# Kernel optimization log

Hardware: AMD Instinct MI355X
Metric: run time of the kernel (lower is better)

## Reference

```python
import jax, jax.numpy as jnp
import numpy as np

B, N, DIM, NUM_NODE = 512, 64, 128, 43098
ALPHA = 0.2          # LeakyReLU negative slope (opt.alpha)
NEG_INF = -9e15      # mask value used by LocalAggregator


def setup_inputs() -> dict:
    key = jax.random.key(0)
    ks = jax.random.split(key, 6)
    stdv = 1.0 / np.sqrt(DIM)
    inputs = jax.random.randint(ks[0], (B, N), 0, NUM_NODE)
    adj = jax.random.randint(ks[1], (B, N, N), 0, 5)          # edge types 0..4
    mask_item = jax.random.randint(ks[2], (B, N), 0, 2)
    item = jax.random.randint(ks[3], (B, N), 0, NUM_NODE)
    embedding = jax.random.uniform(ks[4], (NUM_NODE, DIM), minval=-stdv, maxval=stdv, dtype=jnp.float32)
    attn_a = jax.random.uniform(ks[5], (4, DIM), minval=-stdv, maxval=stdv, dtype=jnp.float32)  # a_0..a_3
    return dict(inputs=inputs, adj=adj, mask_item=mask_item, item=item,
                embedding=embedding, attn_a=attn_a)


def _local_agg(h, adj, attn_a):
    # GCE-GNN LocalAggregator: a_input[b,i,j,:] = h[b,i,:]*h[b,j,:];
    # e_k[b,i,j] = leakyrelu(a_input @ a_k). Computed without materializing
    # the [B,N,N,D] tensor: e_k = leakyrelu(einsum over d of h_i*h_j*a_k).
    e = jax.nn.leaky_relu(jnp.einsum('kd,bid,bjd->kbij', attn_a, h, h), ALPHA)  # [4,B,N,N]
    alpha = jnp.full(e.shape[1:], NEG_INF, dtype=e.dtype)
    for k in range(4):  # edge-type masked selection: adj==k+1 -> e_k
        alpha = jnp.where(adj == k + 1, e[k], alpha)
    alpha = jax.nn.softmax(alpha, axis=-1)          # [B,N,N]
    return jnp.einsum('bij,bjd->bid', alpha, h)     # [B,N,D]


def reference(inputs, adj, mask_item, item, embedding, attn_a):
    h = embedding[inputs]                 # [B,N,D] embedding gather
    h_local = _local_agg(h, adj, attn_a)  # GAT-style local aggregation
    # F.dropout with training=False (eval/inference) is identity
    return h_local
```

## Files before the change

kernel.cpp:

```cpp
#include <hip/hip_runtime.h>
#include <hip/hip_bf16.h>


#define LRELU    0.2f

typedef __bf16 bf16x8 __attribute__((ext_vector_type(8)));
typedef float  f32x4  __attribute__((ext_vector_type(4)));

union FragU { bf16x8 v; unsigned u[4]; uint4 q; };

__device__ __forceinline__ unsigned pk2(float lo, float hi) {
  __hip_bfloat162 t = __float22bfloat162_rn(float2{lo, hi});
  unsigned u;
  __builtin_memcpy(&u, &t, 4);
  return u;
}
__device__ __forceinline__ float bflo(unsigned u) { return __builtin_bit_cast(float, u << 16); }
__device__ __forceinline__ float bfhi(unsigned u) { return __builtin_bit_cast(float, u & 0xffff0000u); }

__global__ __launch_bounds__(512, 4)
void cg_kernel(const int* __restrict__ inputs, const int* __restrict__ adj,
               const float* __restrict__ embedding, const float* __restrict__ attn_a,
               float* __restrict__ out) {
  __shared__ unsigned short Hb[64 * 128];
  __shared__ unsigned short HbT[128 * 64];
  __shared__ unsigned short HA[2][64 * 128];
  __shared__ unsigned short Pl[64 * 64];
  __shared__ float aaL[512];
  __shared__ float redS[64 * 2];

  const int b   = blockIdx.x;
  const int tid = threadIdx.x;
  const int w   = tid >> 6;
  const int l   = tid & 63;
  const int lr  = l & 15;
  const int lg  = l >> 4;
  const int it  = w >> 1;
  const int jh  = w & 1;

  char* HbB  = (char*)Hb;
  char* HbTB = (char*)HbT;
  char* PlB  = (char*)Pl;

  const int row = tid >> 3;
  const int c   = tid & 7;
  const int idx = inputs[b * 64 + row];

  int adjv[2][4];
#pragma unroll
  for (int jt2 = 0; jt2 < 2; ++jt2)
#pragma unroll
    for (int r = 0; r < 4; ++r)
      adjv[jt2][r] = adj[b * 4096 + (16 * it + 4 * lg + r) * 64 + 32 * jh + 16 * jt2 + lr];

  const float4* src = (const float4*)(embedding + (long)idx * 128 + c * 16);
  float4 v0 = src[0], v1 = src[1], v2 = src[2], v3 = src[3];
  aaL[tid] = attn_a[tid];

  unsigned pk[8];
  pk[0] = pk2(v0.x, v0.y); pk[1] = pk2(v0.z, v0.w);
  pk[2] = pk2(v1.x, v1.y); pk[3] = pk2(v1.z, v1.w);
  pk[4] = pk2(v2.x, v2.y); pk[5] = pk2(v2.z, v2.w);
  pk[6] = pk2(v3.x, v3.y); pk[7] = pk2(v3.z, v3.w);
  const int rswz = (row & 7) << 4;
  *(uint4*)(HbB + ((row * 256 + c * 32)      ^ rswz)) = uint4{pk[0], pk[1], pk[2], pk[3]};
  *(uint4*)(HbB + ((row * 256 + c * 32 + 16) ^ rswz)) = uint4{pk[4], pk[5], pk[6], pk[7]};
#pragma unroll
  for (int s = 0; s < 16; ++s) {
    int e = (s + 3 * c) & 15;
    int d = c * 16 + e;
    unsigned short hv = (unsigned short)((e & 1) ? (pk[e >> 1] >> 16) : (pk[e >> 1] & 0xffffu));
    *(unsigned short*)(HbTB + ((d * 128 + row * 2) ^ ((d & 7) << 4))) = hv;
  }
  float hf[16];
#pragma unroll
  for (int e = 0; e < 8; ++e) { hf[2 * e] = bflo(pk[e]); hf[2 * e + 1] = bfhi(pk[e]); }
  __syncthreads();

  uint4 bfrE[2][4];
#pragma unroll
  for (int jt2 = 0; jt2 < 2; ++jt2) {
    int jrow = 16 * (2 * jh + jt2) + lr;
#pragma unroll
    for (int kc = 0; kc < 4; ++kc)
      bfrE[jt2][kc] = *(const uint4*)(HbB + ((jrow * 256 + (kc * 32 + lg * 8) * 2) ^ ((jrow & 7) << 4)));
  }

  {
    float4 a0 = *(const float4*)&aaL[c * 16];
    float4 a1 = *(const float4*)&aaL[c * 16 + 4];
    float4 a2 = *(const float4*)&aaL[c * 16 + 8];
    float4 a3 = *(const float4*)&aaL[c * 16 + 12];
    char* HAB = (char*)HA[0];
    *(uint4*)(HAB + ((row * 256 + c * 32) ^ rswz)) =
        uint4{pk2(hf[0] * a0.x, hf[1] * a0.y),  pk2(hf[2] * a0.z, hf[3] * a0.w),
              pk2(hf[4] * a1.x, hf[5] * a1.y),  pk2(hf[6] * a1.z, hf[7] * a1.w)};
    *(uint4*)(HAB + ((row * 256 + c * 32 + 16) ^ rswz)) =
        uint4{pk2(hf[8] * a2.x,  hf[9] * a2.y),  pk2(hf[10] * a2.z, hf[11] * a2.w),
              pk2(hf[12] * a3.x, hf[13] * a3.y), pk2(hf[14] * a3.z, hf[15] * a3.w)};
  }
  __syncthreads();

  f32x4 acc[4][2];
#pragma unroll
  for (int k = 0; k < 4; ++k)
#pragma unroll
    for (int jt2 = 0; jt2 < 2; ++jt2) acc[k][jt2] = f32x4{0.f, 0.f, 0.f, 0.f};

#pragma unroll
  for (int k = 0; k < 4; ++k) {
    char* HAcur = (char*)HA[k & 1];
    if (k < 3) {
      float4 a0 = *(const float4*)&aaL[(k + 1) * 128 + c * 16];
      float4 a1 = *(const float4*)&aaL[(k + 1) * 128 + c * 16 + 4];
      float4 a2 = *(const float4*)&aaL[(k + 1) * 128 + c * 16 + 8];
      float4 a3 = *(const float4*)&aaL[(k + 1) * 128 + c * 16 + 12];
      char* HAnxt = (char*)HA[(k + 1) & 1];
      *(uint4*)(HAnxt + ((row * 256 + c * 32) ^ rswz)) =
          uint4{pk2(hf[0] * a0.x, hf[1] * a0.y),  pk2(hf[2] * a0.z, hf[3] * a0.w),
                pk2(hf[4] * a1.x, hf[5] * a1.y),  pk2(hf[6] * a1.z, hf[7] * a1.w)};
      *(uint4*)(HAnxt + ((row * 256 + c * 32 + 16) ^ rswz)) =
          uint4{pk2(hf[8] * a2.x,  hf[9] * a2.y),  pk2(hf[10] * a2.z, hf[11] * a2.w),
                pk2(hf[12] * a3.x, hf[13] * a3.y), pk2(hf[14] * a3.z, hf[15] * a3.w)};
    }
#pragma unroll
    for (int kc = 0; kc < 4; ++kc) {
      int arow = 16 * it + lr;
      FragU afr;
      afr.q = *(const uint4*)(HAcur + ((arow * 256 + (kc * 32 + lg * 8) * 2) ^ ((lr & 7) << 4)));
#pragma unroll
      for (int jt2 = 0; jt2 < 2; ++jt2) {
        FragU bfr; bfr.q = bfrE[jt2][kc];
        acc[k][jt2] = __builtin_amdgcn_mfma_f32_16x16x32_bf16(afr.v, bfr.v, acc[k][jt2], 0, 0, 0);
      }
    }
    if (k < 3) __syncthreads();
  }

  float p[2][4];
#pragma unroll
  for (int jt2 = 0; jt2 < 2; ++jt2)
#pragma unroll
    for (int r = 0; r < 4; ++r) {
      int av = adjv[jt2][r];
      float s = acc[0][jt2][r];
      s = (av == 2) ? acc[1][jt2][r] : s;
      s = (av == 3) ? acc[2][jt2][r] : s;
      s = (av == 4) ? acc[3][jt2][r] : s;
      float sl = s > 0.f ? s : LRELU * s;
      p[jt2][r] = (av != 0) ? __expf(sl) : 0.f;
    }
#pragma unroll
  for (int r = 0; r < 4; ++r) {
    int i = 16 * it + 4 * lg + r;
    int iswz = (i & 7) << 4;
    *(unsigned short*)(PlB + ((i * 128 + (32 * jh + lr) * 2)      ^ iswz)) = (unsigned short)(pk2(p[0][r], p[0][r]) & 0xffffu);
    *(unsigned short*)(PlB + ((i * 128 + (32 * jh + 16 + lr) * 2) ^ iswz)) = (unsigned short)(pk2(p[1][r], p[1][r]) & 0xffffu);
    float ss = p[0][r] + p[1][r];
    ss += __shfl_xor(ss, 1);
    ss += __shfl_xor(ss, 2);
    ss += __shfl_xor(ss, 4);
    ss += __shfl_xor(ss, 8);
    if (lr == 0) redS[i * 2 + jh] = ss;
  }
  __syncthreads();
  float z4[4];
#pragma unroll
  for (int r = 0; r < 4; ++r) {
    int i = 16 * it + 4 * lg + r;
    z4[r] = redS[i * 2] + redS[i * 2 + 1];
  }

  FragU afrP[2];
#pragma unroll
  for (int kc2 = 0; kc2 < 2; ++kc2) {
    int prow = 16 * it + lr;
    afrP[kc2].q = *(const uint4*)(PlB + ((prow * 128 + (kc2 * 32 + lg * 8) * 2) ^ ((lr & 7) << 4)));
  }
  f32x4 pv[4];
#pragma unroll
  for (int dtl = 0; dtl < 4; ++dtl) pv[dtl] = f32x4{0.f, 0.f, 0.f, 0.f};
#pragma unroll
  for (int dtl = 0; dtl < 4; ++dtl) {
#pragma unroll
    for (int kc2 = 0; kc2 < 2; ++kc2) {
      int drow = 64 * jh + 16 * dtl + lr;
      FragU bfr;
      bfr.q = *(const uint4*)(HbTB + ((drow * 128 + (kc2 * 32 + lg * 8) * 2) ^ ((drow & 7) << 4)));
      pv[dtl] = __builtin_amdgcn_mfma_f32_16x16x32_bf16(afrP[kc2].v, bfr.v, pv[dtl], 0, 0, 0);
    }
  }

#pragma unroll
  for (int r = 0; r < 4; ++r) {
    int i = 16 * it + 4 * lg + r;
    float invz = 1.0f / z4[r];
#pragma unroll
    for (int dtl = 0; dtl < 4; ++dtl) {
      int d = 64 * jh + 16 * dtl + lr;
      out[(b * 64 + i) * 128 + d] = pv[dtl][r] * invz;
    }
  }
}

extern "C" void kernel_launch(void* const* d_in, const int* in_sizes, int n_in,
                              void* d_out, int out_size, void* d_ws, size_t ws_size,
                              hipStream_t stream) {
  (void)in_sizes; (void)n_in; (void)d_ws; (void)ws_size; (void)out_size;
  const int*   inputs    = (const int*)d_in[0];
  const int*   adj       = (const int*)d_in[1];
  const float* embedding = (const float*)d_in[4];
  const float* attn_a    = (const float*)d_in[5];
  float*       out       = (float*)d_out;
  cg_kernel<<<dim3(512), dim3(512), 0, stream>>>(inputs, adj, embedding, attn_a, out);
}
```

Before: 17.97 us.

## Build attention-scaled A fragments in registers instead of staging through LDS

Removes the double-buffered HA shared-memory arrays and the three per-edge-type barriers. Each wave now reads its raw bf16 H fragment once per k-chunk, scales it in registers by each of the four attention vectors, and feeds the MFMAs directly. This reduces LDS footprint and synchronization, which may allow more blocks per CU. The cost is extra VALU conversion and multiply work per wave, duplicated across the waves that share a row tile.

```diff
diff --git a/kernel.cpp b/kernel.cpp
--- a/kernel.cpp
+++ b/kernel.cpp
@@ -24,7 +24,6 @@
                float* __restrict__ out) {
   __shared__ unsigned short Hb[64 * 128];
   __shared__ unsigned short HbT[128 * 64];
-  __shared__ unsigned short HA[2][64 * 128];
   __shared__ unsigned short Pl[64 * 64];
   __shared__ float aaL[512];
   __shared__ float redS[64 * 2];
@@ -72,33 +71,6 @@
     unsigned short hv = (unsigned short)((e & 1) ? (pk[e >> 1] >> 16) : (pk[e >> 1] & 0xffffu));
     *(unsigned short*)(HbTB + ((d * 128 + row * 2) ^ ((d & 7) << 4))) = hv;
   }
-  float hf[16];
-#pragma unroll
-  for (int e = 0; e < 8; ++e) { hf[2 * e] = bflo(pk[e]); hf[2 * e + 1] = bfhi(pk[e]); }
-  __syncthreads();
-
-  uint4 bfrE[2][4];
-#pragma unroll
-  for (int jt2 = 0; jt2 < 2; ++jt2) {
-    int jrow = 16 * (2 * jh + jt2) + lr;
-#pragma unroll
-    for (int kc = 0; kc < 4; ++kc)
-      bfrE[jt2][kc] = *(const uint4*)(HbB + ((jrow * 256 + (kc * 32 + lg * 8) * 2) ^ ((jrow & 7) << 4)));
-  }
-
-  {
-    float4 a0 = *(const float4*)&aaL[c * 16];
-    float4 a1 = *(const float4*)&aaL[c * 16 + 4];
-    float4 a2 = *(const float4*)&aaL[c * 16 + 8];
-    float4 a3 = *(const float4*)&aaL[c * 16 + 12];
-    char* HAB = (char*)HA[0];
-    *(uint4*)(HAB + ((row * 256 + c * 32) ^ rswz)) =
-        uint4{pk2(hf[0] * a0.x, hf[1] * a0.y),  pk2(hf[2] * a0.z, hf[3] * a0.w),
-              pk2(hf[4] * a1.x, hf[5] * a1.y),  pk2(hf[6] * a1.z, hf[7] * a1.w)};
-    *(uint4*)(HAB + ((row * 256 + c * 32 + 16) ^ rswz)) =
-        uint4{pk2(hf[8] * a2.x,  hf[9] * a2.y),  pk2(hf[10] * a2.z, hf[11] * a2.w),
-              pk2(hf[12] * a3.x, hf[13] * a3.y), pk2(hf[14] * a3.z, hf[15] * a3.w)};
-  }
   __syncthreads();
 
   f32x4 acc[4][2];
@@ -107,34 +79,37 @@
 #pragma unroll
     for (int jt2 = 0; jt2 < 2; ++jt2) acc[k][jt2] = f32x4{0.f, 0.f, 0.f, 0.f};
 
+  const int arow = 16 * it + lr;
+  const int aswz = (lr & 7) << 4;
+
 #pragma unroll
-  for (int k = 0; k < 4; ++k) {
-    char* HAcur = (char*)HA[k & 1];
-    if (k < 3) {
-      float4 a0 = *(const float4*)&aaL[(k + 1) * 128 + c * 16];
-      float4 a1 = *(const float4*)&aaL[(k + 1) * 128 + c * 16 + 4];
-      float4 a2 = *(const float4*)&aaL[(k + 1) * 128 + c * 16 + 8];
-      float4 a3 = *(const float4*)&aaL[(k + 1) * 128 + c * 16 + 12];
-      char* HAnxt = (char*)HA[(k + 1) & 1];
-      *(uint4*)(HAnxt + ((row * 256 + c * 32) ^ rswz)) =
-          uint4{pk2(hf[0] * a0.x, hf[1] * a0.y),  pk2(hf[2] * a0.z, hf[3] * a0.w),
-                pk2(hf[4] * a1.x, hf[5] * a1.y),  pk2(hf[6] * a1.z, hf[7] * a1.w)};
-      *(uint4*)(HAnxt + ((row * 256 + c * 32 + 16) ^ rswz)) =
-          uint4{pk2(hf[8] * a2.x,  hf[9] * a2.y),  pk2(hf[10] * a2.z, hf[11] * a2.w),
-                pk2(hf[12] * a3.x, hf[13] * a3.y), pk2(hf[14] * a3.z, hf[15] * a3.w)};
+  for (int kc = 0; kc < 4; ++kc) {
+    const int dsl = kc * 32 + lg * 8;
+    uint4 ha = *(const uint4*)(HbB + ((arow * 256 + dsl * 2) ^ aswz));
+    float hfa[8];
+    hfa[0] = bflo(ha.x); hfa[1] = bfhi(ha.x);
+    hfa[2] = bflo(ha.y); hfa[3] = bfhi(ha.y);
+    hfa[4] = bflo(ha.z); hfa[5] = bfhi(ha.z);
+    hfa[6] = bflo(ha.w); hfa[7] = bfhi(ha.w);
+    FragU bf0, bf1;
+    {
+      int jr0 = 16 * (2 * jh) + lr;
+      int jr1 = 16 * (2 * jh + 1) + lr;
+      bf0.q = *(const uint4*)(HbB + ((jr0 * 256 + dsl * 2) ^ aswz));
+      bf1.q = *(const uint4*)(HbB + ((jr1 * 256 + dsl * 2) ^ aswz));
     }
 #pragma unroll
-    for (int kc = 0; kc < 4; ++kc) {
-      int arow = 16 * it + lr;
+    for (int k = 0; k < 4; ++k) {
+      float4 a0 = *(const float4*)&aaL[k * 128 + dsl];
+      float4 a1 = *(const float4*)&aaL[k * 128 + dsl + 4];
       FragU afr;
-      afr.q = *(const uint4*)(HAcur + ((arow * 256 + (kc * 32 + lg * 8) * 2) ^ ((lr & 7) << 4)));
-#pragma unroll
-      for (int jt2 = 0; jt2 < 2; ++jt2) {
-        FragU bfr; bfr.q = bfrE[jt2][kc];
-        acc[k][jt2] = __builtin_amdgcn_mfma_f32_16x16x32_bf16(afr.v, bfr.v, acc[k][jt2], 0, 0, 0);
-      }
+      afr.u[0] = pk2(hfa[0] * a0.x, hfa[1] * a0.y);
+      afr.u[1] = pk2(hfa[2] * a0.z, hfa[3] * a0.w);
+      afr.u[2] = pk2(hfa[4] * a1.x, hfa[5] * a1.y);
+      afr.u[3] = pk2(hfa[6] * a1.z, hfa[7] * a1.w);
+      acc[k][0] = __builtin_amdgcn_mfma_f32_16x16x32_bf16(afr.v, bf0.v, acc[k][0], 0, 0, 0);
+      acc[k][1] = __builtin_amdgcn_mfma_f32_16x16x32_bf16(afr.v, bf1.v, acc[k][1], 0, 0, 0);
     }
-    if (k < 3) __syncthreads();
   }
 
   float p[2][4];
@@ -175,7 +150,7 @@
 #pragma unroll
   for (int kc2 = 0; kc2 < 2; ++kc2) {
     int prow = 16 * it + lr;
-    afrP[kc2].q = *(const uint4*)(PlB + ((prow * 128 + (kc2 * 32 + lg * 8) * 2) ^ ((lr & 7) << 4)));
+    afrP[kc2].q = *(const uint4*)(PlB + ((prow * 128 + (kc2 * 32 + lg * 8) * 2) ^ aswz));
   }
   f32x4 pv[4];
 #pragma unroll
```

Result: slower. 18.72 us (+4.1%).
